# Optimization experiments

Hardware: AMD Instinct MI355X
Metric: run time of the kernel (lower is better)

The kernel has to match this reference:

```python
import jax, jax.numpy as jnp
import numpy as np

HEADS = 8
DIM_HEAD = 32
DIM = 256
HIDDEN = HEADS * DIM_HEAD  # 256


def setup_inputs() -> dict:
    key = jax.random.key(0)
    ks = jax.random.split(key, 6)
    B, T, C, H, W = 4, 16, DIM, 32, 32
    x = jax.random.normal(ks[0], (B, T, C, H, W), dtype=jnp.float32)
    rel_pos = jax.random.normal(ks[1], (HEADS, T, T), dtype=jnp.float32)
    # 1x1 conv weights == channel-mixing matrices
    w_qkv = jax.random.normal(ks[2], (3 * HIDDEN, C), dtype=jnp.float32) * (C ** -0.5)
    b_qkv = jnp.zeros((3 * HIDDEN,), dtype=jnp.float32)
    w_out = jax.random.normal(ks[3], (C, HIDDEN), dtype=jnp.float32) * (HIDDEN ** -0.5)
    b_out = jnp.zeros((C,), dtype=jnp.float32)
    return {"x": x, "rel_pos": rel_pos, "w_qkv": w_qkv, "b_qkv": b_qkv,
            "w_out": w_out, "b_out": b_out}


def reference(x, rel_pos, w_qkv, b_qkv, w_out, b_out):
    B, T, C, H, W = x.shape
    scale = DIM_HEAD ** -0.5
    # 1x1 conv QKV projection: (B,T,C,H,W) x (3*hidden, C) -> (B,T,H,W,3*hidden)
    qkv = jnp.einsum('btchw,oc->bthwo', x, w_qkv) + b_qkv
    q, k, v = jnp.split(qkv, 3, axis=-1)
    # split heads: (B,T,H,W,heads,dim_head); attention over T per (b,h,w,head)
    q = q.reshape(B, T, H, W, HEADS, DIM_HEAD) * scale
    k = k.reshape(B, T, H, W, HEADS, DIM_HEAD)
    v = v.reshape(B, T, H, W, HEADS, DIM_HEAD)
    # sim: (B,H,W,heads,T,T)
    sim = jnp.einsum('bihwnd,bjhwnd->bhwnij', q, k)
    sim = sim + rel_pos  # (heads,T,T) broadcasts over (B,H,W)
    attn = jax.nn.softmax(sim, axis=-1)
    out = jnp.einsum('bhwnij,bjhwnd->bihwnd', attn, v)  # (B,T,H,W,heads,dh)
    out = out.reshape(B, T, H, W, HIDDEN)
    # 1x1 conv output projection back to C channels
    y = jnp.einsum('bthwe,ce->bthwc', out, w_out) + b_out
    return jnp.transpose(y, (0, 1, 4, 2, 3))  # (B,T,C,H,W)
```

## Files before the change

### kernel.cpp

```cpp
#include <hip/hip_runtime.h>
#include <hip/hip_bf16.h>

typedef __attribute__((ext_vector_type(8))) short bf16x8;
typedef __attribute__((ext_vector_type(4))) float f32x4;
typedef __attribute__((ext_vector_type(16))) float f32x16;

namespace {

__device__ __forceinline__ unsigned short f2bf(float f) {
  unsigned int x;
  __builtin_memcpy(&x, &f, 4);
  x += 0x7fff + ((x >> 16) & 1);
  return (unsigned short)(x >> 16);
}
__device__ __forceinline__ unsigned int pack2(float a, float b) {
  return (unsigned int)f2bf(a) | ((unsigned int)f2bf(b) << 16);
}

constexpr int kWBStride = 264;
constexpr int kWBTile = 32 * kWBStride;
constexpr int kWB = 2 * kWBTile;
constexpr int kSite = 1824;
constexpr int kSmem = kWB + 8 * kSite;
constexpr int kPanelStride = 72;
constexpr int kWTileOff = 17408;
static_assert(kSmem * 2 <= 65536, "LDS budget");
static_assert(16 * 16 * kPanelStride <= kSmem, "x panel fits");
static_assert(kWTileOff + kWBTile <= kSmem, "wout tile fits after fbuf");

__global__ __launch_bounds__(512, 1) void attn_fused(
    const float* __restrict__ x,
    const float* __restrict__ rel,
    const float* __restrict__ wqkv,
    const float* __restrict__ bqkv,
    const float* __restrict__ wout,
    const float* __restrict__ bout,
    float* __restrict__ out) {
  __shared__ __align__(16) unsigned short smem[kSmem];
  const int tid = threadIdx.x;
  const int lane = tid & 63;
  const int wave = tid >> 6;
  const int quad = lane >> 4;
  const int lrow = lane & 15;
  const int half = lane >> 5;
  const int n32 = lane & 31;
  const int b = blockIdx.x >> 6;
  const int hw0 = (blockIdx.x & 63) * 16;

  const int wrow = tid >> 4;
  const int wcol = (tid & 15) * 16;
  float4 pw[4];
  {
    const float* sp = wqkv + (size_t)wrow * 256 + wcol;
#pragma unroll
    for (int u = 0; u < 4; ++u) pw[u] = *(const float4*)(sp + u * 4);
  }

  bf16x8 ax[16];
  {
    unsigned short* panel = smem;
    const int sloc = wave * 2 + (n32 >> 4);
#pragma unroll
    for (int cc4 = 0; cc4 < 4; ++cc4) {
      const int c0 = cc4 * 64;
      __syncthreads();
#pragma unroll
      for (int u = 0; u < 8; ++u) {
        const int idx = u * 512 + tid;
        const int row = idx >> 2;
        const int q = idx & 3;
        const int t = row >> 6;
        const int cl = row & 63;
        const float4 v = *(const float4*)(
            x + (((size_t)(b * 16 + t) * 256 + c0 + cl) << 10) + hw0 + q * 4);
        unsigned short* pr = panel + (t * 16 + q * 4) * kPanelStride + cl;
        pr[0] = f2bf(v.x);
        pr[kPanelStride] = f2bf(v.y);
        pr[2 * kPanelStride] = f2bf(v.z);
        pr[3 * kPanelStride] = f2bf(v.w);
      }
      __syncthreads();
#pragma unroll
      for (int kk = 0; kk < 4; ++kk)
        ax[cc4 * 4 + kk] = *(const bf16x8*)(
            panel + (lrow * 16 + sloc) * kPanelStride + kk * 16 + half * 8);
    }
  }

  unsigned short* qb = smem + kWB + wave * kSite;
  unsigned short* kb = qb + 640;
  unsigned short* vt = qb + 1280;

  const f32x4 zero4 = {0.f, 0.f, 0.f, 0.f};
  const float scale = 0.17677669529663687f;
  bf16x8 ao[2][8];

  auto qkv_tile = [&](int g, float bias) -> f32x16 {
    __syncthreads();
    unsigned short* WBc = smem + (g & 1) * kWBTile;
    {
      unsigned short* dst = WBc + wrow * kWBStride + wcol;
      uint4 a, bq;
      a.x = pack2(pw[0].x, pw[0].y);
      a.y = pack2(pw[0].z, pw[0].w);
      a.z = pack2(pw[1].x, pw[1].y);
      a.w = pack2(pw[1].z, pw[1].w);
      bq.x = pack2(pw[2].x, pw[2].y);
      bq.y = pack2(pw[2].z, pw[2].w);
      bq.z = pack2(pw[3].x, pw[3].y);
      bq.w = pack2(pw[3].z, pw[3].w);
      *(uint4*)dst = a;
      *(uint4*)(dst + 8) = bq;
    }
    {
      const int gn = g + 1;
      const int rowbase = (gn % 3) * 256 + (gn / 3) * 32;
      const float* sp = wqkv + (size_t)(rowbase + wrow) * 256 + wcol;
#pragma unroll
      for (int u = 0; u < 4; ++u) pw[u] = *(const float4*)(sp + u * 4);
    }
    __syncthreads();
    f32x16 acc;
#pragma unroll
    for (int i = 0; i < 16; ++i) acc[i] = bias;
    const unsigned short* br = WBc + n32 * kWBStride + half * 8;
#pragma unroll
    for (int ks = 0; ks < 16; ++ks) {
      const bf16x8 bf = *(const bf16x8*)(br + ks * 16);
      acc = __builtin_amdgcn_mfma_f32_32x32x16_bf16(ax[ks], bf, acc, 0, 0, 0);
    }
    return acc;
  };

  auto head_body = [&](int h) {
    const f32x16 qacc = qkv_tile(h * 3 + 0, bqkv[h * 32 + n32]);
    const f32x16 kacc = qkv_tile(h * 3 + 1, bqkv[256 + h * 32 + n32]);
    const f32x16 vacc = qkv_tile(h * 3 + 2, bqkv[512 + h * 32 + n32]);
    float rl[4];
#pragma unroll
    for (int r = 0; r < 4; ++r) rl[r] = rel[h * 256 + (quad * 4 + r) * 16 + lrow];

#pragma unroll
    for (int s = 0; s < 2; ++s) {
#pragma unroll
      for (int rr = 0; rr < 8; ++rr) {
        const int t = (rr & 3) + 8 * (rr >> 2) + 4 * half;
        qb[t * 40 + n32] = f2bf(qacc[8 * s + rr]);
        kb[t * 40 + n32] = f2bf(kacc[8 * s + rr]);
      }
#pragma unroll
      for (int rp = 0; rp < 4; ++rp) {
        const int rr = rp * 2;
        const int t = (rr & 3) + 8 * (rr >> 2) + 4 * half;
        *(unsigned int*)&vt[n32 * 16 + t] =
            pack2(vacc[8 * s + rr], vacc[8 * s + rr + 1]);
      }
      const bf16x8 qf = *(const bf16x8*)(qb + lrow * 40 + quad * 8);
      const bf16x8 kf = *(const bf16x8*)(kb + lrow * 40 + quad * 8);
      const f32x4 sim = __builtin_amdgcn_mfma_f32_16x16x32_bf16(qf, kf, zero4, 0, 0, 0);
      float p[4], inv[4];
#pragma unroll
      for (int r = 0; r < 4; ++r) {
        const float v = sim[r] * scale + rl[r];
        float m = v;
        for (int off = 8; off; off >>= 1) m = fmaxf(m, __shfl_xor(m, off));
        const float e = __expf(v - m);
        float sum = e;
        for (int off = 8; off; off >>= 1) sum += __shfl_xor(sum, off);
        p[r] = e;
        inv[r] = 1.0f / sum;
      }
      unsigned short* pb = kb;
#pragma unroll
      for (int r = 0; r < 4; ++r) pb[(quad * 4 + r) * 24 + lrow] = f2bf(p[r]);
      bf16x8 pf, vf0, vf1;
      if (quad < 2) {
        pf = *(const bf16x8*)(pb + lrow * 24 + quad * 8);
        vf0 = *(const bf16x8*)(vt + lrow * 16 + quad * 8);
        vf1 = *(const bf16x8*)(vt + (16 + lrow) * 16 + quad * 8);
      } else {
#pragma unroll
        for (int j = 0; j < 8; ++j) { pf[j] = 0; vf0[j] = 0; vf1[j] = 0; }
      }
      const f32x4 o0 = __builtin_amdgcn_mfma_f32_16x16x32_bf16(pf, vf0, zero4, 0, 0, 0);
      const f32x4 o1 = __builtin_amdgcn_mfma_f32_16x16x32_bf16(pf, vf1, zero4, 0, 0, 0);
#pragma unroll
      for (int r = 0; r < 4; ++r) {
        const int t = quad * 4 + r;
        qb[t * 40 + lrow] = f2bf(o0[r] * inv[r]);
        qb[t * 40 + 16 + lrow] = f2bf(o1[r] * inv[r]);
      }
      ao[s][h] = *(const bf16x8*)(qb + lrow * 40 + quad * 8);
    }
  };

  head_body(0);
  head_body(1);
  head_body(2);
  head_body(3);
  head_body(4);
  head_body(5);
  head_body(6);
  head_body(7);

  __syncthreads();
  float* fbuf = (float*)smem;
  unsigned short* wtile = smem + kWTileOff;
  float* ob = out + ((size_t)b << 22);
#pragma unroll 1
  for (int cc = 0; cc < 8; ++cc) {
    {
      const float* sp = wout + (size_t)(cc * 32 + wrow) * 256 + wcol;
      float4 v0 = ((const float4*)sp)[0];
      float4 v1 = ((const float4*)sp)[1];
      float4 v2 = ((const float4*)sp)[2];
      float4 v3 = ((const float4*)sp)[3];
      uint4 a, bq;
      a.x = pack2(v0.x, v0.y);
      a.y = pack2(v0.z, v0.w);
      a.z = pack2(v1.x, v1.y);
      a.w = pack2(v1.z, v1.w);
      bq.x = pack2(v2.x, v2.y);
      bq.y = pack2(v2.z, v2.w);
      bq.z = pack2(v3.x, v3.y);
      bq.w = pack2(v3.z, v3.w);
      unsigned short* d = wtile + wrow * kWBStride + wcol;
      *(uint4*)d = a;
      *(uint4*)(d + 8) = bq;
    }
    __syncthreads();
#pragma unroll
    for (int sub = 0; sub < 2; ++sub) {
      const int c = cc * 32 + sub * 16 + lrow;
      const float bias = bout[c];
      f32x4 y0 = {bias, bias, bias, bias};
      f32x4 y1 = {bias, bias, bias, bias};
      const unsigned short* wrow_p = wtile + (sub * 16 + lrow) * kWBStride;
#pragma unroll
      for (int ks = 0; ks < 8; ++ks) {
        const bf16x8 wf = *(const bf16x8*)(wrow_p + ks * 32 + quad * 8);
        y0 = __builtin_amdgcn_mfma_f32_16x16x32_bf16(ao[0][ks], wf, y0, 0, 0, 0);
        y1 = __builtin_amdgcn_mfma_f32_16x16x32_bf16(ao[1][ks], wf, y1, 0, 0, 0);
      }
#pragma unroll
      for (int r = 0; r < 4; ++r) {
        const int t = quad * 4 + r;
        const int L = (t * 32 + sub * 16 + lrow) * 17 + wave * 2;
        fbuf[L] = y0[r];
        fbuf[L + 1] = y1[r];
      }
    }
    __syncthreads();
    {
      const int t = tid >> 5, cl = tid & 31;
      float v[16];
#pragma unroll
      for (int i = 0; i < 16; ++i) v[i] = fbuf[tid * 17 + i];
      float* dst = ob + ((size_t)(t * 256 + cc * 32 + cl)) * 1024 + hw0;
#pragma unroll
      for (int u = 0; u < 4; ++u) {
        float4 q;
        q.x = v[u * 4]; q.y = v[u * 4 + 1]; q.z = v[u * 4 + 2]; q.w = v[u * 4 + 3];
        *(float4*)(dst + u * 4) = q;
      }
    }
    __syncthreads();
  }
}

}

extern "C" void kernel_launch(void* const* d_in, const int* in_sizes, int n_in,
                              void* d_out, int out_size, void* d_ws, size_t ws_size,
                              hipStream_t stream) {
  const float* x = (const float*)d_in[0];
  const float* rel = (const float*)d_in[1];
  const float* wqkv = (const float*)d_in[2];
  const float* bqkv = (const float*)d_in[3];
  const float* wout = (const float*)d_in[4];
  const float* bout = (const float*)d_in[5];
  float* out = (float*)d_out;
  (void)in_sizes; (void)n_in; (void)out_size; (void)d_ws; (void)ws_size;

  attn_fused<<<256, 512, 0, stream>>>(x, rel, wqkv, bqkv, wout, bout, out);
}
```

Before: 196.9 us.

## Stage Q/K/V weight tiles per head together to cut block barriers

The weights for Q, K and V of one head are now staged together into a double-buffered group of three tiles, instead of one tile per projection. This cuts the block-wide barriers from six per head to two. Prefetched weights are kept in registers already packed to bf16, and the per-wave scratch buffers are enlarged so both s-halves of Q/K/V are written before the attention step. The cost is a much larger LDS allocation, beyond 64 KiB, which depends on the 160 KiB per-CU LDS, and more live registers for the packed prefetch.

```diff
diff --git a/kernel.cpp b/kernel.cpp
--- a/kernel.cpp
+++ b/kernel.cpp
@@ -19,13 +19,13 @@
 
 constexpr int kWBStride = 264;
 constexpr int kWBTile = 32 * kWBStride;
-constexpr int kWB = 2 * kWBTile;
-constexpr int kSite = 1824;
-constexpr int kSmem = kWB + 8 * kSite;
+constexpr int kWG = 3 * kWBTile;
+constexpr int kSite = 3584;
+constexpr int kSmem = 2 * kWG + 8 * kSite;
 constexpr int kPanelStride = 72;
 constexpr int kWTileOff = 17408;
-static_assert(kSmem * 2 <= 65536, "LDS budget");
-static_assert(16 * 16 * kPanelStride <= kSmem, "x panel fits");
+static_assert(kSmem * 2 <= 160 * 1024, "LDS within 160KiB/CU");
+static_assert(16 * 16 * kPanelStride <= kWG, "x panel fits in WG0");
 static_assert(kWTileOff + kWBTile <= kSmem, "wout tile fits after fbuf");
 
 __global__ __launch_bounds__(512, 1) void attn_fused(
@@ -49,12 +49,21 @@
 
   const int wrow = tid >> 4;
   const int wcol = (tid & 15) * 16;
-  float4 pw[4];
-  {
-    const float* sp = wqkv + (size_t)wrow * 256 + wcol;
-#pragma unroll
-    for (int u = 0; u < 4; ++u) pw[u] = *(const float4*)(sp + u * 4);
-  }
+  uint4 pwp[6];
+  auto loadpack = [&](int g, uint4& lo, uint4& hi) {
+    const int rowbase = (g % 3) * 256 + (g / 3) * 32;
+    const float* sp = wqkv + (size_t)(rowbase + wrow) * 256 + wcol;
+    const float4 v0 = ((const float4*)sp)[0];
+    const float4 v1 = ((const float4*)sp)[1];
+    const float4 v2 = ((const float4*)sp)[2];
+    const float4 v3 = ((const float4*)sp)[3];
+    lo.x = pack2(v0.x, v0.y); lo.y = pack2(v0.z, v0.w);
+    lo.z = pack2(v1.x, v1.y); lo.w = pack2(v1.z, v1.w);
+    hi.x = pack2(v2.x, v2.y); hi.y = pack2(v2.z, v2.w);
+    hi.z = pack2(v3.x, v3.y); hi.w = pack2(v3.z, v3.w);
+  };
+#pragma unroll
+  for (int u = 0; u < 3; ++u) loadpack(u, pwp[2 * u], pwp[2 * u + 1]);
 
   bf16x8 ax[16];
   {
@@ -87,43 +96,20 @@
     }
   }
 
-  unsigned short* qb = smem + kWB + wave * kSite;
-  unsigned short* kb = qb + 640;
-  unsigned short* vt = qb + 1280;
-
+  unsigned short* qb = smem + 2 * kWG + wave * kSite;
+  unsigned short* kb = qb + 1280;
+  unsigned short* vt = qb + 2560;
+
+  const int stageDst = wrow * kWBStride + wcol;
   const f32x4 zero4 = {0.f, 0.f, 0.f, 0.f};
   const float scale = 0.17677669529663687f;
   bf16x8 ao[2][8];
 
-  auto qkv_tile = [&](int g, float bias) -> f32x16 {
-    __syncthreads();
-    unsigned short* WBc = smem + (g & 1) * kWBTile;
-    {
-      unsigned short* dst = WBc + wrow * kWBStride + wcol;
-      uint4 a, bq;
-      a.x = pack2(pw[0].x, pw[0].y);
-      a.y = pack2(pw[0].z, pw[0].w);
-      a.z = pack2(pw[1].x, pw[1].y);
-      a.w = pack2(pw[1].z, pw[1].w);
-      bq.x = pack2(pw[2].x, pw[2].y);
-      bq.y = pack2(pw[2].z, pw[2].w);
-      bq.z = pack2(pw[3].x, pw[3].y);
-      bq.w = pack2(pw[3].z, pw[3].w);
-      *(uint4*)dst = a;
-      *(uint4*)(dst + 8) = bq;
-    }
-    {
-      const int gn = g + 1;
-      const int rowbase = (gn % 3) * 256 + (gn / 3) * 32;
-      const float* sp = wqkv + (size_t)(rowbase + wrow) * 256 + wcol;
-#pragma unroll
-      for (int u = 0; u < 4; ++u) pw[u] = *(const float4*)(sp + u * 4);
-    }
-    __syncthreads();
+  auto mfma16 = [&](const unsigned short* WT, float bias) -> f32x16 {
     f32x16 acc;
 #pragma unroll
     for (int i = 0; i < 16; ++i) acc[i] = bias;
-    const unsigned short* br = WBc + n32 * kWBStride + half * 8;
+    const unsigned short* br = WT + n32 * kWBStride + half * 8;
 #pragma unroll
     for (int ks = 0; ks < 16; ++ks) {
       const bf16x8 bf = *(const bf16x8*)(br + ks * 16);
@@ -132,31 +118,63 @@
     return acc;
   };
 
-  auto head_body = [&](int h) {
-    const f32x16 qacc = qkv_tile(h * 3 + 0, bqkv[h * 32 + n32]);
-    const f32x16 kacc = qkv_tile(h * 3 + 1, bqkv[256 + h * 32 + n32]);
-    const f32x16 vacc = qkv_tile(h * 3 + 2, bqkv[512 + h * 32 + n32]);
+  auto head_phase = [&](int h) {
+    __syncthreads();
+    unsigned short* WGc = smem + (h & 1) * kWG;
+#pragma unroll
+    for (int u = 0; u < 3; ++u) {
+      *(uint4*)(WGc + u * kWBTile + stageDst) = pwp[2 * u];
+      *(uint4*)(WGc + u * kWBTile + stageDst + 8) = pwp[2 * u + 1];
+    }
+#pragma unroll
+    for (int u = 0; u < 3; ++u) {
+      int gt = 3 * (h + 1) + u;
+      if (gt > 23) gt = 23;
+      loadpack(gt, pwp[2 * u], pwp[2 * u + 1]);
+    }
+    __syncthreads();
+
+    {
+      const f32x16 qacc = mfma16(WGc, bqkv[h * 32 + n32]);
+#pragma unroll
+      for (int s = 0; s < 2; ++s)
+#pragma unroll
+        for (int rr = 0; rr < 8; ++rr) {
+          const int t = (rr & 3) + 8 * (rr >> 2) + 4 * half;
+          qb[s * 640 + t * 40 + n32] = f2bf(qacc[8 * s + rr]);
+        }
+    }
+    {
+      const f32x16 kacc = mfma16(WGc + kWBTile, bqkv[256 + h * 32 + n32]);
+#pragma unroll
+      for (int s = 0; s < 2; ++s)
+#pragma unroll
+        for (int rr = 0; rr < 8; ++rr) {
+          const int t = (rr & 3) + 8 * (rr >> 2) + 4 * half;
+          kb[s * 640 + t * 40 + n32] = f2bf(kacc[8 * s + rr]);
+        }
+    }
+    {
+      const f32x16 vacc = mfma16(WGc + 2 * kWBTile, bqkv[512 + h * 32 + n32]);
+#pragma unroll
+      for (int s = 0; s < 2; ++s)
+#pragma unroll
+        for (int rp = 0; rp < 4; ++rp) {
+          const int rr = rp * 2;
+          const int t = (rr & 3) + 8 * (rr >> 2) + 4 * half;
+          *(unsigned int*)&vt[s * 512 + n32 * 16 + t] =
+              pack2(vacc[8 * s + rr], vacc[8 * s + rr + 1]);
+        }
+    }
+
     float rl[4];
 #pragma unroll
     for (int r = 0; r < 4; ++r) rl[r] = rel[h * 256 + (quad * 4 + r) * 16 + lrow];
 
 #pragma unroll
     for (int s = 0; s < 2; ++s) {
-#pragma unroll
-      for (int rr = 0; rr < 8; ++rr) {
-        const int t = (rr & 3) + 8 * (rr >> 2) + 4 * half;
-        qb[t * 40 + n32] = f2bf(qacc[8 * s + rr]);
-        kb[t * 40 + n32] = f2bf(kacc[8 * s + rr]);
-      }
-#pragma unroll
-      for (int rp = 0; rp < 4; ++rp) {
-        const int rr = rp * 2;
-        const int t = (rr & 3) + 8 * (rr >> 2) + 4 * half;
-        *(unsigned int*)&vt[n32 * 16 + t] =
-            pack2(vacc[8 * s + rr], vacc[8 * s + rr + 1]);
-      }
-      const bf16x8 qf = *(const bf16x8*)(qb + lrow * 40 + quad * 8);
-      const bf16x8 kf = *(const bf16x8*)(kb + lrow * 40 + quad * 8);
+      const bf16x8 qf = *(const bf16x8*)(qb + s * 640 + lrow * 40 + quad * 8);
+      const bf16x8 kf = *(const bf16x8*)(kb + s * 640 + lrow * 40 + quad * 8);
       const f32x4 sim = __builtin_amdgcn_mfma_f32_16x16x32_bf16(qf, kf, zero4, 0, 0, 0);
       float p[4], inv[4];
 #pragma unroll
@@ -170,14 +188,14 @@
         p[r] = e;
         inv[r] = 1.0f / sum;
       }
-      unsigned short* pb = kb;
+      unsigned short* pb = kb + s * 640;
 #pragma unroll
       for (int r = 0; r < 4; ++r) pb[(quad * 4 + r) * 24 + lrow] = f2bf(p[r]);
       bf16x8 pf, vf0, vf1;
       if (quad < 2) {
         pf = *(const bf16x8*)(pb + lrow * 24 + quad * 8);
-        vf0 = *(const bf16x8*)(vt + lrow * 16 + quad * 8);
-        vf1 = *(const bf16x8*)(vt + (16 + lrow) * 16 + quad * 8);
+        vf0 = *(const bf16x8*)(vt + s * 512 + lrow * 16 + quad * 8);
+        vf1 = *(const bf16x8*)(vt + s * 512 + (16 + lrow) * 16 + quad * 8);
       } else {
 #pragma unroll
         for (int j = 0; j < 8; ++j) { pf[j] = 0; vf0[j] = 0; vf1[j] = 0; }
@@ -187,21 +205,21 @@
 #pragma unroll
       for (int r = 0; r < 4; ++r) {
         const int t = quad * 4 + r;
-        qb[t * 40 + lrow] = f2bf(o0[r] * inv[r]);
-        qb[t * 40 + 16 + lrow] = f2bf(o1[r] * inv[r]);
-      }
-      ao[s][h] = *(const bf16x8*)(qb + lrow * 40 + quad * 8);
+        qb[s * 640 + t * 40 + lrow] = f2bf(o0[r] * inv[r]);
+        qb[s * 640 + t * 40 + 16 + lrow] = f2bf(o1[r] * inv[r]);
+      }
+      ao[s][h] = *(const bf16x8*)(qb + s * 640 + lrow * 40 + quad * 8);
     }
   };
 
-  head_body(0);
-  head_body(1);
-  head_body(2);
-  head_body(3);
-  head_body(4);
-  head_body(5);
-  head_body(6);
-  head_body(7);
+  head_phase(0);
+  head_phase(1);
+  head_phase(2);
+  head_phase(3);
+  head_phase(4);
+  head_phase(5);
+  head_phase(6);
+  head_phase(7);
 
   __syncthreads();
   float* fbuf = (float*)smem;
@@ -211,10 +229,10 @@
   for (int cc = 0; cc < 8; ++cc) {
     {
       const float* sp = wout + (size_t)(cc * 32 + wrow) * 256 + wcol;
-      float4 v0 = ((const float4*)sp)[0];
-      float4 v1 = ((const float4*)sp)[1];
-      float4 v2 = ((const float4*)sp)[2];
-      float4 v3 = ((const float4*)sp)[3];
+      const float4 v0 = ((const float4*)sp)[0];
+      const float4 v1 = ((const float4*)sp)[1];
+      const float4 v2 = ((const float4*)sp)[2];
+      const float4 v3 = ((const float4*)sp)[3];
       uint4 a, bq;
       a.x = pack2(v0.x, v0.y);
       a.y = pack2(v0.z, v0.w);
```

Result: slower. 206.3 us (+4.7%).
